# Kernel tuning notes

Hardware: AMD Instinct MI355X
Metric: run time of the kernel (lower is better)

The kernel has to match this reference:

```python
import jax, jax.numpy as jnp
import numpy as np
import math

D = 1024            # model dim
H = 4               # gru heads
HD = D // H         # 256 head dim
DI = int(HD * 1.5)  # 384 minGRU inner dim (expansion_factor=1.5)
FF_INNER = int(D * 4 * 2 / 3)  # 2730 SwiGLU inner
K = 4               # causal depthwise conv kernel
RES_SCALE = 1.0     # 1/sqrt(num_layers=1)


def setup_inputs() -> dict:
    key = jax.random.key(0)
    ks = jax.random.split(key, 12)
    s = lambda k, shape, sc: jax.random.normal(k, shape, jnp.float32) * sc
    return {
        "x": s(ks[0], (4, 4096, D), 1.0),
        "dw_w": s(ks[1], (D, 1, K), 0.3),
        "dw_b": jnp.zeros((D,), jnp.float32),
        "pw_w": s(ks[2], (D, D), 1.0 / math.sqrt(D)),
        "pw_b": jnp.zeros((D,), jnp.float32),
        "conv_gamma": jnp.zeros((D,), jnp.float32),
        "gru_gamma": jnp.zeros((D,), jnp.float32),
        "ff_gamma": jnp.zeros((D,), jnp.float32),
        "w_hg": s(ks[3], (H, HD, 2 * DI), 1.0 / math.sqrt(HD)),
        "w_out": s(ks[4], (H, DI, HD), 1.0 / math.sqrt(DI)),
        "w_gate": s(ks[5], (D, FF_INNER), 1.0 / math.sqrt(D)),
        "w_value": s(ks[6], (D, FF_INNER), 1.0 / math.sqrt(D)),
        "w_ff_out": s(ks[7], (FF_INNER, D), 1.0 / math.sqrt(FF_INNER)),
    }


def _rmsnorm(x, gamma):
    # F.normalize(x, dim=-1) * sqrt(dim) * (gamma + 1)
    n = jnp.sqrt(jnp.sum(x * x, axis=-1, keepdims=True))
    return x / jnp.maximum(n, 1e-12) * math.sqrt(x.shape[-1]) * (gamma + 1.0)


def _log_g(x):
    return jnp.where(x >= 0, jnp.log(jax.nn.relu(x) + 0.5), -jax.nn.softplus(-x))


def _causal_conv(x, dw_w, dw_b, pw_w, pw_b):
    # x: [B,L,D] -> causal depthwise conv (k=K) -> pointwise 1x1
    xt = jnp.transpose(x, (0, 2, 1))  # [B,D,L]
    xt = jnp.pad(xt, ((0, 0), (0, 0), (K - 1, 0)))
    y = jax.lax.conv_general_dilated(
        xt, dw_w, (1,), "VALID",
        dimension_numbers=("NCH", "OIH", "NCH"),
        feature_group_count=D) + dw_b[None, :, None]
    y = jnp.einsum("bdl,ed->bel", y, pw_w) + pw_b[None, :, None]
    return jnp.transpose(y, (0, 2, 1))


def reference(x, dw_w, dw_b, pw_w, pw_b, conv_gamma, gru_gamma, ff_gamma,
              w_hg, w_out, w_gate, w_value, w_ff_out):
    B, L, _ = x.shape
    # conv residual branch
    x = _causal_conv(_rmsnorm(x, conv_gamma), dw_w, dw_b, pw_w, pw_b) * RES_SCALE + x
    # multi-head minGRU (all heads vectorized; prev_hidden=None)
    normed = _rmsnorm(x, gru_gamma).reshape(B, L, H, HD)
    hg = jnp.einsum("blhd,hde->blhe", normed, w_hg)  # [B,L,H,2*DI]
    hidden, gate = hg[..., :DI], hg[..., DI:]
    log_coeffs = -jax.nn.softplus(gate)
    log_values = -jax.nn.softplus(-gate) + _log_g(hidden)
    # heinsen associative scan in log space along L
    a_star = jnp.cumsum(log_coeffs, axis=1)
    log_h = a_star + jax.lax.cumlogsumexp(log_values - a_star, axis=1)
    h = jnp.exp(log_h)  # [B,L,H,DI]
    next_hidden = h[:, -1:].reshape(B, 1, H * DI)
    gru_out = jnp.einsum("blhe,heo->blho", h, w_out).reshape(B, L, D)
    x = gru_out * RES_SCALE + x
    # SwiGLU FFN residual branch
    n = _rmsnorm(x, ff_gamma)
    ff = (jax.nn.silu(n @ w_gate) * (n @ w_value)) @ w_ff_out
    x = ff * RES_SCALE + x
    return x, next_hidden
```

## Files before the change

kernel.cpp:

```cpp
#include <hip/hip_runtime.h>
#include <stdint.h>


#define DM     1024
#define SEQL   4096
#define FFN    2730
#define FFP    2816
#define NH_OFF 16777216L
#define CHLEN  128

using bf16x8 = __attribute__((ext_vector_type(8))) short;
using f32x4  = __attribute__((ext_vector_type(4))) float;

__device__ __forceinline__ float bf2f(unsigned short h) {
  union { unsigned int u; float f; } v; v.u = ((unsigned int)h) << 16; return v.f;
}
__device__ __forceinline__ unsigned short f2bf(float f) {
  union { float f; unsigned int u; } v; v.f = f;
  unsigned int u = v.u;
  return (unsigned short)((u + 0x7fffu + ((u >> 16) & 1u)) >> 16);
}
__device__ __forceinline__ float ldin(const void* p, long i, int f32mode) {
  return f32mode ? ((const float*)p)[i] : bf2f(((const unsigned short*)p)[i]);
}
__device__ __forceinline__ void stout(void* p, long i, int f32mode, float v) {
  if (f32mode) ((float*)p)[i] = v; else ((unsigned short*)p)[i] = f2bf(v);
}
__device__ __forceinline__ void gload_lds16(const unsigned short* g, unsigned short* lds) {
  __builtin_amdgcn_global_load_lds(
      (const __attribute__((address_space(1))) unsigned int*)g,
      (__attribute__((address_space(3))) unsigned int*)lds,
      16, 0, 0);
}

__global__ void detect_k(const unsigned short* __restrict__ x, int* __restrict__ flag) {
  __shared__ int cnt;
  if (threadIdx.x == 0) cnt = 0;
  __syncthreads();
  int c = 0;
  for (int j = 0; j < 4; j++) {
    unsigned short v = x[2 * (threadIdx.x * 4 + j)];
    int ex = (v >> 7) & 0xFF;
    if (ex >= 0x84) c++;
  }
  atomicAdd(&cnt, c);
  __syncthreads();
  if (threadIdx.x == 0) *flag = (cnt >= 32) ? 1 : 0;
}

template <int EPI>
__launch_bounds__(256)
__global__ void gemm_bf16(const unsigned short* __restrict__ A, int lda, int aOffZ,
                          const unsigned short* __restrict__ Bm, int bOffZ, int K,
                          void* __restrict__ Cout, int ldc, int cOffZ, long outOff,
                          const unsigned short* __restrict__ bias,
                          const void* __restrict__ res, int ldres, long resOff,
                          const int* __restrict__ flagp) {
  __shared__ __align__(16) unsigned short As[128][64];
  __shared__ __align__(16) unsigned short Bs[128][64];

  const int tid  = threadIdx.x;
  const int w    = tid >> 6;
  const int lane = tid & 63;
  const int z    = blockIdx.z;
  const long tm  = (long)blockIdx.y * 128;
  const long tn  = (long)blockIdx.x * 128;

  const unsigned short* Ag = A + (long)z * aOffZ;
  const unsigned short* Bg = Bm + (long)z * bOffZ;

  f32x4 acc[4][4];
#pragma unroll
  for (int i = 0; i < 4; i++)
#pragma unroll
    for (int j = 0; j < 4; j++) acc[i][j] = (f32x4){0.f, 0.f, 0.f, 0.f};

  const int wrow = w * 32;
  const int srow = lane >> 3;
  const int scol = (((lane & 7) ^ srow) * 8);
  const int wm   = (w >> 1) * 64;
  const int wn   = (w & 1) * 64;
  const int quad = lane >> 4;
  const int lo   = lane & 15;
  const int sw   = lo & 7;

  for (int k0 = 0; k0 < K; k0 += 64) {
    __syncthreads();
#pragma unroll
    for (int i = 0; i < 4; i++) {
      const int r = wrow + i * 8;
      gload_lds16(Ag + (tm + r + srow) * (long)lda + k0 + scol, &As[r][0]);
      gload_lds16(Bg + (tn + r + srow) * (long)K + k0 + scol, &Bs[r][0]);
    }
    __syncthreads();
#pragma unroll
    for (int kk = 0; kk < 64; kk += 32) {
      const int kc = kk >> 3;
      bf16x8 af[4], bfr[4];
#pragma unroll
      for (int mt = 0; mt < 4; mt++)
        af[mt] = *(const bf16x8*)&As[wm + mt * 16 + lo][((quad + kc) ^ sw) * 8];
#pragma unroll
      for (int nt = 0; nt < 4; nt++)
        bfr[nt] = *(const bf16x8*)&Bs[wn + nt * 16 + lo][((quad + kc) ^ sw) * 8];
#pragma unroll
      for (int mt = 0; mt < 4; mt++)
#pragma unroll
        for (int nt = 0; nt < 4; nt++)
          acc[mt][nt] = __builtin_amdgcn_mfma_f32_16x16x32_bf16(af[mt], bfr[nt], acc[mt][nt], 0, 0, 0);
    }
  }

  const int f32m = (EPI == 1 || EPI == 3) ? *flagp : 0;
#pragma unroll
  for (int mt = 0; mt < 4; mt++) {
#pragma unroll
    for (int nt = 0; nt < 4; nt++) {
#pragma unroll
      for (int r = 0; r < 4; r++) {
        const long grow = tm + wm + mt * 16 + quad * 4 + r;
        const long gcol = tn + wn + nt * 16 + lo;
        float v         = acc[mt][nt][r];
        if (EPI == 0) {
          ((unsigned short*)Cout + (long)z * cOffZ)[grow * (long)ldc + gcol] = f2bf(v);
        } else if (EPI == 1) {
          v += bf2f(bias[gcol]) + ldin(res, resOff + grow * (long)ldres + gcol, f32m);
          ((unsigned short*)Cout)[grow * (long)ldc + gcol] = f2bf(v);
        } else if (EPI == 2) {
          v += bf2f(((const unsigned short*)res + (long)z * cOffZ)[grow * (long)ldres + gcol]);
          ((unsigned short*)Cout + (long)z * cOffZ)[grow * (long)ldc + gcol] = f2bf(v);
        } else {
          v += bf2f(((const unsigned short*)res)[grow * (long)ldres + gcol]);
          stout(Cout, outOff + grow * (long)ldc + gcol, f32m, v);
        }
      }
    }
  }
}

__launch_bounds__(256)
__global__ void gemm_ff(const unsigned short* __restrict__ A,
                        const unsigned short* __restrict__ Bgm,
                        const unsigned short* __restrict__ Bvm,
                        unsigned short* __restrict__ Cout) {
  __shared__ __align__(16) unsigned short As[128][64];
  __shared__ __align__(16) unsigned short Bgs[128][64];
  __shared__ __align__(16) unsigned short Bvs[128][64];

  const int tid  = threadIdx.x;
  const int w    = tid >> 6;
  const int lane = tid & 63;
  const long tm  = (long)blockIdx.y * 128;
  const long tn  = (long)blockIdx.x * 128;

  f32x4 accG[4][4], accV[4][4];
#pragma unroll
  for (int i = 0; i < 4; i++)
#pragma unroll
    for (int j = 0; j < 4; j++) {
      accG[i][j] = (f32x4){0.f, 0.f, 0.f, 0.f};
      accV[i][j] = (f32x4){0.f, 0.f, 0.f, 0.f};
    }

  const int wrow = w * 32;
  const int srow = lane >> 3;
  const int scol = (((lane & 7) ^ srow) * 8);
  const int wm   = (w >> 1) * 64;
  const int wn   = (w & 1) * 64;
  const int quad = lane >> 4;
  const int lo   = lane & 15;
  const int sw   = lo & 7;

  for (int k0 = 0; k0 < DM; k0 += 64) {
    __syncthreads();
#pragma unroll
    for (int i = 0; i < 4; i++) {
      const int r = wrow + i * 8;
      gload_lds16(A + (tm + r + srow) * (long)DM + k0 + scol, &As[r][0]);
      gload_lds16(Bgm + (tn + r + srow) * (long)DM + k0 + scol, &Bgs[r][0]);
      gload_lds16(Bvm + (tn + r + srow) * (long)DM + k0 + scol, &Bvs[r][0]);
    }
    __syncthreads();
#pragma unroll
    for (int kk = 0; kk < 64; kk += 32) {
      const int kc = kk >> 3;
      bf16x8 af[4], bfr[4];
#pragma unroll
      for (int mt = 0; mt < 4; mt++)
        af[mt] = *(const bf16x8*)&As[wm + mt * 16 + lo][((quad + kc) ^ sw) * 8];
#pragma unroll
      for (int nt = 0; nt < 4; nt++)
        bfr[nt] = *(const bf16x8*)&Bgs[wn + nt * 16 + lo][((quad + kc) ^ sw) * 8];
#pragma unroll
      for (int mt = 0; mt < 4; mt++)
#pragma unroll
        for (int nt = 0; nt < 4; nt++)
          accG[mt][nt] = __builtin_amdgcn_mfma_f32_16x16x32_bf16(af[mt], bfr[nt], accG[mt][nt], 0, 0, 0);
#pragma unroll
      for (int nt = 0; nt < 4; nt++)
        bfr[nt] = *(const bf16x8*)&Bvs[wn + nt * 16 + lo][((quad + kc) ^ sw) * 8];
#pragma unroll
      for (int mt = 0; mt < 4; mt++)
#pragma unroll
        for (int nt = 0; nt < 4; nt++)
          accV[mt][nt] = __builtin_amdgcn_mfma_f32_16x16x32_bf16(af[mt], bfr[nt], accV[mt][nt], 0, 0, 0);
    }
  }

#pragma unroll
  for (int mt = 0; mt < 4; mt++) {
#pragma unroll
    for (int nt = 0; nt < 4; nt++) {
#pragma unroll
      for (int r = 0; r < 4; r++) {
        const long grow = tm + wm + mt * 16 + quad * 4 + r;
        const long gcol = tn + wn + nt * 16 + lo;
        const float g   = accG[mt][nt][r];
        const float s   = g / (1.f + __expf(-g));
        Cout[grow * (long)FFP + gcol] = f2bf(s * accV[mt][nt][r]);
      }
    }
  }
}

template <int EPI>
__launch_bounds__(512, 2)
__global__ void gemm256(const unsigned short* __restrict__ A,
                        const unsigned short* __restrict__ Bm,
                        int K,
                        void* __restrict__ Cout,
                        const unsigned short* __restrict__ res,
                        long outOff,
                        const int* __restrict__ flagp) {
  __shared__ __align__(16) unsigned short As[2][256][64];
  __shared__ __align__(16) unsigned short Bs[2][256][64];

  const int tid  = threadIdx.x;
  const int w    = tid >> 6;
  const int lane = tid & 63;
  const int wr   = w >> 2;
  const int wc   = w & 3;
  const int quad = lane >> 4;
  const int lo   = lane & 15;
  const int sw   = lo & 7;

  const int gx  = gridDim.x;
  int bid       = blockIdx.y * gx + blockIdx.x;
  const int nwg = gx * gridDim.y;
  {
    const int q = nwg >> 3, r8 = nwg & 7;
    const int xc8 = bid & 7, j = bid >> 3;
    bid = (xc8 < r8 ? xc8 * (q + 1) : r8 * (q + 1) + (xc8 - r8) * q) + j;
  }
  const long tn = (long)(bid % gx) * 256;
  const long tm = (long)(bid / gx) * 256;

  const int NT = K >> 6;

  const int srow = lane >> 3;
  const int sch  = (lane & 7) ^ srow;
  const unsigned short* Ab = A + (tm + (long)w * 8 + srow) * (long)K + sch * 8;
  const unsigned short* Bb = Bm + (tn + (long)w * 8 + srow) * (long)K + sch * 8;

#define STAGE_A(BUF, TT, G) \
  gload_lds16(Ab + (long)((G) * 64) * K + (long)(TT) * 64, &As[BUF][(G) * 64 + w * 8][0])
#define STAGE_B(BUF, TT, G) \
  gload_lds16(Bb + (long)((G) * 64) * K + (long)(TT) * 64, &Bs[BUF][(G) * 64 + w * 8][0])

  STAGE_A(0, 0, 0); STAGE_A(0, 0, 2);
  STAGE_A(0, 0, 1); STAGE_A(0, 0, 3);
  STAGE_B(0, 0, 0); STAGE_B(0, 0, 1); STAGE_B(0, 0, 2); STAGE_B(0, 0, 3);
  STAGE_A(1, 1, 0); STAGE_A(1, 1, 2);
  STAGE_A(1, 1, 1); STAGE_A(1, 1, 3);
  STAGE_B(1, 1, 0); STAGE_B(1, 1, 1); STAGE_B(1, 1, 2); STAGE_B(1, 1, 3);

  f32x4 acc[8][4];
#pragma unroll
  for (int i = 0; i < 8; i++)
#pragma unroll
    for (int j = 0; j < 4; j++) acc[i][j] = (f32x4){0.f, 0.f, 0.f, 0.f};

  asm volatile("s_waitcnt vmcnt(8)" ::: "memory");
  __builtin_amdgcn_s_barrier();

  bf16x8 aL[4][2], aH[4][2], b01[2][2], b23[2][2];

#define LDAL(CBUF)                                                                \
  _Pragma("unroll") for (int m = 0; m < 4; m++) {                                 \
    _Pragma("unroll") for (int c = 0; c < 2; c++) {                               \
      aL[m][c] = *(const bf16x8*)&As[CBUF][wr * 128 + m * 16 + lo]                \
                                        [((quad + 4 * c) ^ sw) * 8];              \
    }                                                                             \
  }
#define LDAH(CBUF)                                                                \
  _Pragma("unroll") for (int m = 0; m < 4; m++) {                                 \
    _Pragma("unroll") for (int c = 0; c < 2; c++) {                               \
      aH[m][c] = *(const bf16x8*)&As[CBUF][wr * 128 + 64 + m * 16 + lo]           \
                                        [((quad + 4 * c) ^ sw) * 8];              \
    }                                                                             \
  }
#define LDB01(CBUF)                                                               \
  _Pragma("unroll") for (int n = 0; n < 2; n++) {                                 \
    _Pragma("unroll") for (int c = 0; c < 2; c++) {                               \
      b01[n][c] = *(const bf16x8*)&Bs[CBUF][wc * 64 + n * 16 + lo]                \
                                         [((quad + 4 * c) ^ sw) * 8];             \
    }                                                                             \
  }
#define LDB23(CBUF)                                                               \
  _Pragma("unroll") for (int n = 0; n < 2; n++) {                                 \
    _Pragma("unroll") for (int c = 0; c < 2; c++) {                               \
      b23[n][c] = *(const bf16x8*)&Bs[CBUF][wc * 64 + 32 + n * 16 + lo]           \
                                         [((quad + 4 * c) ^ sw) * 8];             \
    }                                                                             \
  }
#define MFMA_Q(MB, AF, NB, BF)                                                    \
  __builtin_amdgcn_s_setprio(1);                                                  \
  _Pragma("unroll") for (int m = 0; m < 4; m++) {                                 \
    _Pragma("unroll") for (int n = 0; n < 2; n++) {                               \
      _Pragma("unroll") for (int c = 0; c < 2; c++) {                             \
        acc[(MB) + m][(NB) + n] = __builtin_amdgcn_mfma_f32_16x16x32_bf16(        \
            AF[m][c], BF[n][c], acc[(MB) + m][(NB) + n], 0, 0, 0);                \
      }                                                                           \
    }                                                                             \
  }                                                                               \
  __builtin_amdgcn_s_setprio(0);

#define LGKM0 asm volatile("s_waitcnt lgkmcnt(0)" ::: "memory")

#define SUBTILE(CBUF, TT, STG, PRF, VM)                                           \
  {                                                                               \
                                                            \
    LGKM0;                                                                        \
    if (STG) { STAGE_A(CBUF, (TT) + 2, 0); STAGE_A(CBUF, (TT) + 2, 2); }          \
    MFMA_Q(0, aL, 0, b01);                                                        \
    LDAH(CBUF);                                                                   \
    __builtin_amdgcn_s_barrier();                                                 \
                                                            \
    LGKM0;                                                                        \
    if (STG) { STAGE_A(CBUF, (TT) + 2, 1); STAGE_A(CBUF, (TT) + 2, 3); }          \
    MFMA_Q(4, aH, 0, b01);                                                        \
    LDB23(CBUF);                                                                  \
    if ((VM) == 4) asm volatile("s_waitcnt vmcnt(4)" ::: "memory");               \
    else if ((VM) == 0) asm volatile("s_waitcnt vmcnt(0)" ::: "memory");          \
    __builtin_amdgcn_s_barrier();                                                 \
                                                            \
    LGKM0;                                                                        \
    if (STG) { STAGE_B(CBUF, (TT) + 2, 0); STAGE_B(CBUF, (TT) + 2, 1);            \
               STAGE_B(CBUF, (TT) + 2, 2); STAGE_B(CBUF, (TT) + 2, 3); }          \
    MFMA_Q(0, aL, 2, b23);                                                        \
    if (PRF) LDB01(CBUF ^ 1);                                                     \
    __builtin_amdgcn_s_barrier();                                                 \
                        \
    MFMA_Q(4, aH, 2, b23);                                                        \
    if (PRF) LDAL(CBUF ^ 1);                                                      \
    __builtin_amdgcn_s_barrier();                                                 \
  }

  LDB01(0);
  LDAL(0);

  for (int t = 0; t + 3 < NT; t += 2) {
    SUBTILE(0, t, 1, 1, 4)
    SUBTILE(1, t + 1, 1, 1, 4)
  }
  SUBTILE(0, NT - 2, 0, 1, 0)
  SUBTILE(1, NT - 1, 0, 0, -1)

  if (EPI == 0) {
    const long colb = (tn >> 1);
    const long rowb = tm + wr * 128;
#pragma unroll
    for (int m = 0; m < 8; m++) {
#pragma unroll
      for (int np = 0; np < 2; np++) {
        const long col = colb + (wc * 2 + np) * 16 + lo;
#pragma unroll
        for (int r = 0; r < 4; r++) {
          const long row = rowb + m * 16 + quad * 4 + r;
          const float g  = acc[m][2 * np][r];
          const float v  = acc[m][2 * np + 1][r];
          const float s  = g / (1.f + __expf(-g));
          ((unsigned short*)Cout)[row * (long)FFP + col] = f2bf(s * v);
        }
      }
    }
  } else {
    const int f32m = *flagp;
    const long rowb = tm + wr * 128;
    const long colb = tn + wc * 64;
#pragma unroll
    for (int m = 0; m < 8; m++) {
#pragma unroll
      for (int n = 0; n < 4; n++) {
#pragma unroll
        for (int r = 0; r < 4; r++) {
          const long row = rowb + m * 16 + quad * 4 + r;
          const long col = colb + n * 16 + lo;
          float v = acc[m][n][r] + bf2f(res[row * (long)DM + col]);
          stout(Cout, outOff + row * (long)DM + col, f32m, v);
        }
      }
    }
  }
#undef STAGE_A
#undef STAGE_B
#undef LDAL
#undef LDAH
#undef LDB01
#undef LDB23
#undef MFMA_Q
#undef LGKM0
#undef SUBTILE
}

__global__ void rmsnorm_x(const void* __restrict__ in, long elemOff,
                          const unsigned short* __restrict__ gamma,
                          unsigned short* __restrict__ out,
                          const int* __restrict__ flagp) {
  const int t    = blockIdx.x;
  const int lane = threadIdx.x;
  const int f32m = *flagp;
  float v[16];
  const long base = elemOff + (long)t * DM;
  if (f32m) {
    const float4* rp = (const float4*)((const float*)in + base);
#pragma unroll
    for (int j = 0; j < 4; j++) {
      float4 u     = rp[j * 64 + lane];
      v[j * 4 + 0] = u.x; v[j * 4 + 1] = u.y; v[j * 4 + 2] = u.z; v[j * 4 + 3] = u.w;
    }
  } else {
    const ushort4* rp = (const ushort4*)((const unsigned short*)in + base);
#pragma unroll
    for (int j = 0; j < 4; j++) {
      ushort4 u    = rp[j * 64 + lane];
      v[j * 4 + 0] = bf2f(u.x); v[j * 4 + 1] = bf2f(u.y);
      v[j * 4 + 2] = bf2f(u.z); v[j * 4 + 3] = bf2f(u.w);
    }
  }
  float s = 0.f;
#pragma unroll
  for (int i = 0; i < 16; i++) s = fmaf(v[i], v[i], s);
#pragma unroll
  for (int off = 32; off > 0; off >>= 1) s += __shfl_xor(s, off, 64);
  const float scale = 32.f / fmaxf(sqrtf(s), 1e-12f);
  ushort4* op       = (ushort4*)(out + (long)t * DM);
  const ushort4* gp = (const ushort4*)gamma;
#pragma unroll
  for (int j = 0; j < 4; j++) {
    ushort4 g = gp[j * 64 + lane];
    ushort4 o;
    o.x = f2bf(v[j * 4 + 0] * scale * (bf2f(g.x) + 1.f));
    o.y = f2bf(v[j * 4 + 1] * scale * (bf2f(g.y) + 1.f));
    o.z = f2bf(v[j * 4 + 2] * scale * (bf2f(g.z) + 1.f));
    o.w = f2bf(v[j * 4 + 3] * scale * (bf2f(g.w) + 1.f));
    op[j * 64 + lane] = o;
  }
}

__global__ void rmsnorm_k(const unsigned short* __restrict__ in,
                          const unsigned short* __restrict__ gamma,
                          unsigned short* __restrict__ out) {
  const int t    = blockIdx.x;
  const int lane = threadIdx.x;
  float v[16];
  const ushort4* rp = (const ushort4*)(in + (long)t * DM);
#pragma unroll
  for (int j = 0; j < 4; j++) {
    ushort4 u    = rp[j * 64 + lane];
    v[j * 4 + 0] = bf2f(u.x); v[j * 4 + 1] = bf2f(u.y);
    v[j * 4 + 2] = bf2f(u.z); v[j * 4 + 3] = bf2f(u.w);
  }
  float s = 0.f;
#pragma unroll
  for (int i = 0; i < 16; i++) s = fmaf(v[i], v[i], s);
#pragma unroll
  for (int off = 32; off > 0; off >>= 1) s += __shfl_xor(s, off, 64);
  const float scale = 32.f / fmaxf(sqrtf(s), 1e-12f);
  ushort4* op       = (ushort4*)(out + (long)t * DM);
  const ushort4* gp = (const ushort4*)gamma;
#pragma unroll
  for (int j = 0; j < 4; j++) {
    ushort4 g = gp[j * 64 + lane];
    ushort4 o;
    o.x = f2bf(v[j * 4 + 0] * scale * (bf2f(g.x) + 1.f));
    o.y = f2bf(v[j * 4 + 1] * scale * (bf2f(g.y) + 1.f));
    o.z = f2bf(v[j * 4 + 2] * scale * (bf2f(g.z) + 1.f));
    o.w = f2bf(v[j * 4 + 3] * scale * (bf2f(g.w) + 1.f));
    op[j * 64 + lane] = o;
  }
}

__global__ void dwconv_k(const unsigned short* __restrict__ xn,
                         const unsigned short* __restrict__ dww,
                         const unsigned short* __restrict__ dwb,
                         unsigned short* __restrict__ y, int l0) {
  const int t = blockIdx.x;
  const int d = blockIdx.y * 256 + threadIdx.x;
  const int l = l0 + (t & (SEQL - 1));
  ushort4 w4  = ((const ushort4*)dww)[d];
  float wk[4] = {bf2f(w4.x), bf2f(w4.y), bf2f(w4.z), bf2f(w4.w)};
  float acc   = bf2f(dwb[d]);
#pragma unroll
  for (int k = 0; k < 4; k++) {
    const int ll = l + k - 3;
    if (ll >= 0) acc = fmaf(bf2f(xn[(long)(t + k - 3) * DM + d]), wk[k], acc);
  }
  y[(long)t * DM + d] = f2bf(acc);
}

__device__ __forceinline__ void cv_compute(float gt, float& c, float& sg) {
  gt = fminf(fmaxf(gt, -40.f), 40.f);
  const float e  = __expf(-fabsf(gt));
  const float r  = 1.f / (1.f + e);
  const float rs = e * r;
  c  = (gt >= 0.f) ? rs : r;
  sg = (gt >= 0.f) ? r : rs;
}
__device__ __forceinline__ float gfun(float hid) {
  hid = fminf(fmaxf(hid, -40.f), 40.f);
  if (hid >= 0.f) return hid + 0.5f;
  const float e = __expf(hid);
  return e / (1.f + e);
}

__global__ void scan_p1(const unsigned short* __restrict__ hg, float* __restrict__ cC,
                        float* __restrict__ cV, int chTot, int SL) {
  const int e = threadIdx.x, bh = blockIdx.y, cid = blockIdx.x;
  const int bL = bh >> 2, hh = bh & 3;
  long base = ((long)(bL * SL + cid * CHLEN)) * 3072 + hh * 768 + e;
  float C = 1.f, V = 0.f;
  for (int i = 0; i < CHLEN; i++) {
    const float hid = bf2f(hg[base]), gt = bf2f(hg[base + 384]);
    float c, sg; cv_compute(gt, c, sg);
    C *= c;
    V = fmaf(c, V, sg * gfun(hid));
    base += 3072;
  }
  const int idx = cid * chTot + bh * 384 + e;
  cC[idx] = C; cV[idx] = V;
}

__global__ void scan_p2(const float* __restrict__ cC, const float* __restrict__ cV,
                        float* __restrict__ hin, int chTot, int CHNp,
                        const float* __restrict__ hcarry, int useCarry) {
  const int ch = blockIdx.x * 384 + threadIdx.x;
  float h = useCarry ? hcarry[ch] : 0.f;
  for (int cid = 0; cid < CHNp; cid++) {
    const int idx = cid * chTot + ch;
    hin[idx] = h;
    h = fmaf(cC[idx], h, cV[idx]);
  }
}

__global__ void scan_p3(const unsigned short* __restrict__ hg, const float* __restrict__ hin,
                        unsigned short* __restrict__ hout, void* __restrict__ nh, long nhOff,
                        float* __restrict__ hcarry, int chTot, int SL, int CHNp,
                        int writeNh, const int* __restrict__ flagp) {
  const int e = threadIdx.x, bh = blockIdx.y, cid = blockIdx.x;
  const int bL = bh >> 2, hh = bh & 3;
  const long tok = (long)bL * SL + (long)cid * CHLEN;
  long base  = tok * 3072 + hh * 768 + e;
  long obase = tok * 1536 + hh * 384 + e;
  float h = hin[cid * chTot + bh * 384 + e];
  for (int i = 0; i < CHLEN; i++) {
    const float hid = bf2f(hg[base]), gt = bf2f(hg[base + 384]);
    float c, sg; cv_compute(gt, c, sg);
    h = fmaf(c, h, sg * gfun(hid));
    hout[obase] = f2bf(h);
    base += 3072; obase += 1536;
  }
  if (cid == CHNp - 1) {
    hcarry[bh * 384 + e] = h;
    if (writeNh) stout(nh, nhOff + bL * 1536 + hh * 384 + e, *flagp, h);
  }
}

__global__ void cvt_k(const void* __restrict__ in, unsigned short* __restrict__ out,
                      int n, const int* __restrict__ flagp) {
  const int i = blockIdx.x * 256 + threadIdx.x;
  if (i < n) out[i] = f2bf(ldin(in, i, *flagp));
}
__global__ void tr_whg(const void* __restrict__ in, unsigned short* __restrict__ out,
                       const int* __restrict__ flagp) {
  const int idx = blockIdx.x * 256 + threadIdx.x;
  const int k = idx & 255, n = (idx >> 8) % 768, h = idx / (768 * 256);
  out[idx] = f2bf(ldin(in, (long)(h * 256 + k) * 768 + n, *flagp));
}
__global__ void tr_wout(const void* __restrict__ in, unsigned short* __restrict__ out,
                        const int* __restrict__ flagp) {
  const int idx = blockIdx.x * 256 + threadIdx.x;
  const int k = idx % 384, n = (idx / 384) & 255, h = idx / (384 * 256);
  out[idx] = f2bf(ldin(in, (long)(h * 384 + k) * 256 + n, *flagp));
}
__global__ void tr_wg(const void* __restrict__ in, unsigned short* __restrict__ out,
                      const int* __restrict__ flagp) {
  const int idx = blockIdx.x * 256 + threadIdx.x;
  const int k = idx & 1023, n = idx >> 10;
  out[idx] = (n < FFN) ? f2bf(ldin(in, (long)k * FFN + n, *flagp)) : (unsigned short)0;
}
__global__ void tr_wgv(const void* __restrict__ wg, const void* __restrict__ wv,
                       unsigned short* __restrict__ out, const int* __restrict__ flagp) {
  const int idx = blockIdx.x * 256 + threadIdx.x;
  const int k = idx & 1023, R = idx >> 10;
  const int tile = R >> 8, rb = R & 255;
  const int pair = rb >> 5, sel = (rb >> 4) & 1, r16 = rb & 15;
  const int col  = tile * 128 + pair * 16 + r16;
  const void* src = sel ? wv : wg;
  out[idx] = (col < FFN) ? f2bf(ldin(src, (long)k * FFN + col, *flagp)) : (unsigned short)0;
}
__global__ void tr_wfo(const void* __restrict__ in, unsigned short* __restrict__ out,
                       const int* __restrict__ flagp) {
  const int idx = blockIdx.x * 256 + threadIdx.x;
  const int kk = idx % FFP, n = idx / FFP;
  out[idx] = (kk < FFN) ? f2bf(ldin(in, (long)kk * DM + n, *flagp)) : (unsigned short)0;
}

extern "C" void kernel_launch(void* const* d_in, const int* in_sizes, int n_in,
                              void* d_out, int out_size, void* d_ws, size_t ws_size,
                              hipStream_t stream) {
  const void* x      = d_in[0];
  const void* dw_w   = d_in[1];
  const void* dw_b   = d_in[2];
  const void* pw_w   = d_in[3];
  const void* pw_b   = d_in[4];
  const void* conv_g = d_in[5];
  const void* gru_g  = d_in[6];
  const void* ff_g   = d_in[7];
  const void* w_hg   = d_in[8];
  const void* w_out  = d_in[9];
  const void* w_gate = d_in[10];
  const void* w_val  = d_in[11];
  const void* w_ffo  = d_in[12];

  const long FIXED = 21795072L;
  int MT = 128;
  if      (ws_size >= (size_t)(FIXED + 16384L * 13888)) MT = 16384;
  else if (ws_size >= (size_t)(FIXED + 8192L * 13888))  MT = 8192;
  else if (ws_size >= (size_t)(FIXED + 4096L * 13888))  MT = 4096;
  else if (ws_size >= (size_t)(FIXED + 2048L * 13888))  MT = 2048;
  else if (ws_size >= (size_t)(FIXED + 1024L * 13888))  MT = 1024;
  else if (ws_size >= (size_t)(FIXED + 512L * 13888))   MT = 512;
  else if (ws_size >= (size_t)(FIXED + 256L * 13888))   MT = 256;

  const int SL    = (MT >= SEQL) ? SEQL : MT;
  const int nSeq  = MT / SL;
  const int CHNp  = SL / CHLEN;
  const int chTot = nSeq * 1536;
  const int big   = (MT >= 256);

  char* p = (char*)d_ws;
  unsigned short* whgT  = (unsigned short*)p; p += 1572864;
  unsigned short* woutT = (unsigned short*)p; p += 786432;
  unsigned short* wgT   = (unsigned short*)p; p += 5767168;
  unsigned short* wvT   = (unsigned short*)p; p += 5767168;
  unsigned short* wfoT  = (unsigned short*)p; p += 5767168;
  unsigned short* pwT   = (unsigned short*)p; p += 2097152;
  unsigned short* dwwB  = (unsigned short*)p; p += 8192;
  unsigned short* dwbB  = (unsigned short*)p; p += 2048;
  unsigned short* pwbB  = (unsigned short*)p; p += 2048;
  unsigned short* cgB   = (unsigned short*)p; p += 2048;
  unsigned short* ggB   = (unsigned short*)p; p += 2048;
  unsigned short* fgB   = (unsigned short*)p; p += 2048;
  int*            flag  = (int*)p;            p += 256;
  float*          hcarry= (float*)p;          p += 12288;
  float*          cC    = (float*)p;          p += (long)MT * 192;
  float*          cV    = (float*)p;          p += (long)MT * 192;
  float*          hin   = (float*)p;          p += (long)MT * 192;
  unsigned short* xnb   = (unsigned short*)p; p += 6144 + (long)MT * 2048;
  unsigned short* xc    = (unsigned short*)p; p += (long)MT * 2048;
  unsigned short* hbuf  = (unsigned short*)p; p += (long)MT * 3072;
  unsigned short* ybuf  = (unsigned short*)p;
  unsigned short* hg    = (unsigned short*)p;
  unsigned short* ffin  = (unsigned short*)p;
  unsigned short* xn    = xnb + 3 * DM;
  unsigned short* wgvT  = wgT;

  detect_k<<<1, 256, 0, stream>>>((const unsigned short*)x, flag);
  tr_whg<<<3072, 256, 0, stream>>>(w_hg, whgT, flag);
  tr_wout<<<1536, 256, 0, stream>>>(w_out, woutT, flag);
  if (big) {
    tr_wgv<<<22528, 256, 0, stream>>>(w_gate, w_val, wgvT, flag);
  } else {
    tr_wg<<<11264, 256, 0, stream>>>(w_gate, wgT, flag);
    tr_wg<<<11264, 256, 0, stream>>>(w_val, wvT, flag);
  }
  tr_wfo<<<11264, 256, 0, stream>>>(w_ffo, wfoT, flag);
  cvt_k<<<4096, 256, 0, stream>>>(pw_w, pwT, 1048576, flag);
  cvt_k<<<16, 256, 0, stream>>>(dw_w, dwwB, 4096, flag);
  cvt_k<<<4, 256, 0, stream>>>(dw_b, dwbB, 1024, flag);
  cvt_k<<<4, 256, 0, stream>>>(pw_b, pwbB, 1024, flag);
  cvt_k<<<4, 256, 0, stream>>>(conv_g, cgB, 1024, flag);
  cvt_k<<<4, 256, 0, stream>>>(gru_g, ggB, 1024, flag);
  cvt_k<<<4, 256, 0, stream>>>(ff_g, fgB, 1024, flag);

  for (long t0 = 0; t0 < 16384; t0 += MT) {
    const int l0     = (int)(t0 & (SEQL - 1));
    const int P      = (l0 > 0) ? 3 : 0;
    const int seqEnd = (l0 + SL == SEQL);
    const long nhOff = NH_OFF + (t0 / SEQL) * 1536;

    rmsnorm_x<<<MT + P, 64, 0, stream>>>(x, (t0 - P) * DM, cgB, xn - (long)P * DM, flag);
    dwconv_k<<<dim3(MT, 4), 256, 0, stream>>>(xn, dwwB, dwbB, ybuf, l0);
    gemm_bf16<1><<<dim3(8, MT / 128, 1), 256, 0, stream>>>(ybuf, DM, 0, pwT, 0, DM,
        xc, DM, 0, 0L, pwbB, x, DM, t0 * DM, flag);

    rmsnorm_k<<<MT, 64, 0, stream>>>(xc, ggB, xn);
    gemm_bf16<0><<<dim3(6, MT / 128, 4), 256, 0, stream>>>(xn, DM, 256, whgT, 196608, 256,
        hg, 3072, 768, 0L, nullptr, nullptr, 0, 0L, nullptr);
    scan_p1<<<dim3(CHNp, nSeq * 4), 384, 0, stream>>>(hg, cC, cV, chTot, SL);
    scan_p2<<<nSeq * 4, 384, 0, stream>>>(cC, cV, hin, chTot, CHNp, hcarry, l0 > 0);
    scan_p3<<<dim3(CHNp, nSeq * 4), 384, 0, stream>>>(hg, hin, hbuf, d_out, nhOff,
        hcarry, chTot, SL, CHNp, seqEnd, flag);
    gemm_bf16<2><<<dim3(2, MT / 128, 4), 256, 0, stream>>>(hbuf, 1536, 384, woutT, 98304, 384,
        xc, DM, 256, 0L, nullptr, xc, DM, 0L, nullptr);

    rmsnorm_k<<<MT, 64, 0, stream>>>(xc, fgB, xn);
    if (big) {
      gemm256<0><<<dim3(22, MT / 256), 512, 0, stream>>>(xn, wgvT, DM,
          ffin, nullptr, 0L, nullptr);
      gemm256<1><<<dim3(4, MT / 256), 512, 0, stream>>>(ffin, wfoT, FFP,
          d_out, xc, t0 * DM, flag);
    } else {
      gemm_ff<<<dim3(22, MT / 128), 256, 0, stream>>>(xn, wgT, wvT, ffin);
      gemm_bf16<3><<<dim3(8, MT / 128, 1), 256, 0, stream>>>(ffin, FFP, 0, wfoT, 0, FFP,
          d_out, DM, 0, t0 * DM, nullptr, xc, DM, 0L, flag);
    }
  }
}
```

Before: 1.063 ms.

## Restructure GEMM subtile schedule: reorder LDS loads, staging and MFMA quadrants

Reworks the inner-loop schedule of the 256x256 bf16 GEMM. The cross-subtile register prefetch of the next buffer's A/B fragments and the explicit lgkmcnt(0) waits are removed. LDS fragment loads are now issued at the start of each subtile, B and A global->LDS staging are each grouped into one phase, and the vmcnt wait threshold is changed to 8. The aim is cleaner overlap of global staging with MFMA, but dropping the register prefetch exposes more LDS latency at subtile starts, and removing the explicit waits puts correctness at the mercy of compiler-inserted waits.

Measured after the change: 966.4 us. 1.1x faster.

```diff
diff --git a/kernel.cpp b/kernel.cpp
--- a/kernel.cpp
+++ b/kernel.cpp
@@ -267,12 +267,10 @@
 #define STAGE_B(BUF, TT, G) \
   gload_lds16(Bb + (long)((G) * 64) * K + (long)(TT) * 64, &Bs[BUF][(G) * 64 + w * 8][0])
 
-  STAGE_A(0, 0, 0); STAGE_A(0, 0, 2);
-  STAGE_A(0, 0, 1); STAGE_A(0, 0, 3);
+  STAGE_A(0, 0, 0); STAGE_A(0, 0, 1); STAGE_A(0, 0, 2); STAGE_A(0, 0, 3);
   STAGE_B(0, 0, 0); STAGE_B(0, 0, 1); STAGE_B(0, 0, 2); STAGE_B(0, 0, 3);
-  STAGE_A(1, 1, 0); STAGE_A(1, 1, 2);
-  STAGE_A(1, 1, 1); STAGE_A(1, 1, 3);
   STAGE_B(1, 1, 0); STAGE_B(1, 1, 1); STAGE_B(1, 1, 2); STAGE_B(1, 1, 3);
+  STAGE_A(1, 1, 0); STAGE_A(1, 1, 1); STAGE_A(1, 1, 2); STAGE_A(1, 1, 3);
 
   f32x4 acc[8][4];
 #pragma unroll
@@ -325,46 +323,38 @@
   }                                                                               \
   __builtin_amdgcn_s_setprio(0);
 
-#define LGKM0 asm volatile("s_waitcnt lgkmcnt(0)" ::: "memory")
-
-#define SUBTILE(CBUF, TT, STG, PRF, VM)                                           \
+#define SUBTILE(CBUF, TT, STG, VM)                                                \
   {                                                                               \
-                                                            \
-    LGKM0;                                                                        \
-    if (STG) { STAGE_A(CBUF, (TT) + 2, 0); STAGE_A(CBUF, (TT) + 2, 2); }          \
+         \
+    LDAL(CBUF);                                                                   \
+    LDB01(CBUF);                                                                  \
     MFMA_Q(0, aL, 0, b01);                                                        \
+    LDB23(CBUF);                                                                  \
+    __builtin_amdgcn_s_barrier();                                                 \
+                      \
+    MFMA_Q(0, aL, 2, b23);                                                        \
+    __builtin_amdgcn_s_barrier();                                                 \
+         \
+    if (STG) { STAGE_B(CBUF, (TT) + 2, 0); STAGE_B(CBUF, (TT) + 2, 1);            \
+               STAGE_B(CBUF, (TT) + 2, 2); STAGE_B(CBUF, (TT) + 2, 3); }          \
     LDAH(CBUF);                                                                   \
+    MFMA_Q(4, aH, 2, b23);                                                        \
     __builtin_amdgcn_s_barrier();                                                 \
-                                                            \
-    LGKM0;                                                                        \
-    if (STG) { STAGE_A(CBUF, (TT) + 2, 1); STAGE_A(CBUF, (TT) + 2, 3); }          \
+         \
+    if (STG) { STAGE_A(CBUF, (TT) + 2, 0); STAGE_A(CBUF, (TT) + 2, 1);            \
+               STAGE_A(CBUF, (TT) + 2, 2); STAGE_A(CBUF, (TT) + 2, 3); }          \
     MFMA_Q(4, aH, 0, b01);                                                        \
-    LDB23(CBUF);                                                                  \
-    if ((VM) == 4) asm volatile("s_waitcnt vmcnt(4)" ::: "memory");               \
+    if ((VM) == 8) asm volatile("s_waitcnt vmcnt(8)" ::: "memory");               \
     else if ((VM) == 0) asm volatile("s_waitcnt vmcnt(0)" ::: "memory");          \
     __builtin_amdgcn_s_barrier();                                                 \
-                                                            \
-    LGKM0;                                                                        \
-    if (STG) { STAGE_B(CBUF, (TT) + 2, 0); STAGE_B(CBUF, (TT) + 2, 1);            \
-               STAGE_B(CBUF, (TT) + 2, 2); STAGE_B(CBUF, (TT) + 2, 3); }          \
-    MFMA_Q(0, aL, 2, b23);                                                        \
-    if (PRF) LDB01(CBUF ^ 1);                                                     \
-    __builtin_amdgcn_s_barrier();                                                 \
-                        \
-    MFMA_Q(4, aH, 2, b23);                                                        \
-    if (PRF) LDAL(CBUF ^ 1);                                                      \
-    __builtin_amdgcn_s_barrier();                                                 \
-  }
-
-  LDB01(0);
-  LDAL(0);
+  }
 
   for (int t = 0; t + 3 < NT; t += 2) {
-    SUBTILE(0, t, 1, 1, 4)
-    SUBTILE(1, t + 1, 1, 1, 4)
-  }
-  SUBTILE(0, NT - 2, 0, 1, 0)
-  SUBTILE(1, NT - 1, 0, 0, -1)
+    SUBTILE(0, t, 1, 8)
+    SUBTILE(1, t + 1, 1, 8)
+  }
+  SUBTILE(0, NT - 2, 0, 0)
+  SUBTILE(1, NT - 1, 0, -1)
 
   if (EPI == 0) {
     const long colb = (tn >> 1);
@@ -409,7 +399,6 @@
 #undef LDB01
 #undef LDB23
 #undef MFMA_Q
-#undef LGKM0
 #undef SUBTILE
 }
 
```

## Reschedule GEMM main-loop phases to interleave LDS reads with MFMA

Applied to the files above, without the earlier changes.

Reorders the four-phase schedule of the bf16 MFMA GEMM main loop. Both B fragment halves are now loaded up front, the A-high fragment loads are split into two halves spread across phases, and the global-to-LDS staging of each buffer region is moved to phases where no wave still reads it. The explicit lgkmcnt(0) waits are replaced by sched_barrier plus s_barrier phase boundaries, and the prologue issue order and vmcnt thresholds are adjusted to match. The aim is to hide LDS read latency behind MFMA work. This relies on the compiler to insert the LDS waits and raises register pressure from holding more fragments at once.

After: 1.056 ms. No clear change (-0.7%).

```diff
diff --git a/kernel.cpp b/kernel.cpp
--- a/kernel.cpp
+++ b/kernel.cpp
@@ -268,11 +268,11 @@
   gload_lds16(Bb + (long)((G) * 64) * K + (long)(TT) * 64, &Bs[BUF][(G) * 64 + w * 8][0])
 
   STAGE_A(0, 0, 0); STAGE_A(0, 0, 2);
+  STAGE_B(0, 0, 0); STAGE_B(0, 0, 1); STAGE_B(0, 0, 2); STAGE_B(0, 0, 3);
   STAGE_A(0, 0, 1); STAGE_A(0, 0, 3);
-  STAGE_B(0, 0, 0); STAGE_B(0, 0, 1); STAGE_B(0, 0, 2); STAGE_B(0, 0, 3);
   STAGE_A(1, 1, 0); STAGE_A(1, 1, 2);
+  STAGE_B(1, 1, 0); STAGE_B(1, 1, 1); STAGE_B(1, 1, 2); STAGE_B(1, 1, 3);
   STAGE_A(1, 1, 1); STAGE_A(1, 1, 3);
-  STAGE_B(1, 1, 0); STAGE_B(1, 1, 1); STAGE_B(1, 1, 2); STAGE_B(1, 1, 3);
 
   f32x4 acc[8][4];
 #pragma unroll
@@ -292,8 +292,15 @@
                                         [((quad + 4 * c) ^ sw) * 8];              \
     }                                                                             \
   }
-#define LDAH(CBUF)                                                                \
-  _Pragma("unroll") for (int m = 0; m < 4; m++) {                                 \
+#define LDAH1(CBUF)                                                               \
+  _Pragma("unroll") for (int m = 0; m < 2; m++) {                                 \
+    _Pragma("unroll") for (int c = 0; c < 2; c++) {                               \
+      aH[m][c] = *(const bf16x8*)&As[CBUF][wr * 128 + 64 + m * 16 + lo]           \
+                                        [((quad + 4 * c) ^ sw) * 8];              \
+    }                                                                             \
+  }
+#define LDAH2(CBUF)                                                               \
+  _Pragma("unroll") for (int m = 2; m < 4; m++) {                                 \
     _Pragma("unroll") for (int c = 0; c < 2; c++) {                               \
       aH[m][c] = *(const bf16x8*)&As[CBUF][wr * 128 + 64 + m * 16 + lo]           \
                                         [((quad + 4 * c) ^ sw) * 8];              \
@@ -325,43 +332,46 @@
   }                                                                               \
   __builtin_amdgcn_s_setprio(0);
 
-#define LGKM0 asm volatile("s_waitcnt lgkmcnt(0)" ::: "memory")
+#define PHASE_END                                                                 \
+  __builtin_amdgcn_sched_barrier(0);                                              \
+  __builtin_amdgcn_s_barrier();
 
 #define SUBTILE(CBUF, TT, STG, PRF, VM)                                           \
   {                                                                               \
-                                                            \
-    LGKM0;                                                                        \
+     \
+     \
+    LDB01(CBUF);                                                                  \
+    LDB23(CBUF);                                                                  \
+    MFMA_Q(0, aL, 0, b01);                                                        \
+    PHASE_END;                                                                    \
+     \
+     \
     if (STG) { STAGE_A(CBUF, (TT) + 2, 0); STAGE_A(CBUF, (TT) + 2, 2); }          \
-    MFMA_Q(0, aL, 0, b01);                                                        \
-    LDAH(CBUF);                                                                   \
-    __builtin_amdgcn_s_barrier();                                                 \
-                                                            \
-    LGKM0;                                                                        \
-    if (STG) { STAGE_A(CBUF, (TT) + 2, 1); STAGE_A(CBUF, (TT) + 2, 3); }          \
-    MFMA_Q(4, aH, 0, b01);                                                        \
-    LDB23(CBUF);                                                                  \
-    if ((VM) == 4) asm volatile("s_waitcnt vmcnt(4)" ::: "memory");               \
-    else if ((VM) == 0) asm volatile("s_waitcnt vmcnt(0)" ::: "memory");          \
-    __builtin_amdgcn_s_barrier();                                                 \
-                                                            \
-    LGKM0;                                                                        \
+    LDAH1(CBUF);                                                                  \
+    MFMA_Q(0, aL, 2, b23);                                                        \
+    PHASE_END;                                                                    \
+     \
+     \
     if (STG) { STAGE_B(CBUF, (TT) + 2, 0); STAGE_B(CBUF, (TT) + 2, 1);            \
                STAGE_B(CBUF, (TT) + 2, 2); STAGE_B(CBUF, (TT) + 2, 3); }          \
-    MFMA_Q(0, aL, 2, b23);                                                        \
-    if (PRF) LDB01(CBUF ^ 1);                                                     \
-    __builtin_amdgcn_s_barrier();                                                 \
-                        \
+    LDAH2(CBUF);                                                                  \
     MFMA_Q(4, aH, 2, b23);                                                        \
+    if ((VM) == 6) asm volatile("s_waitcnt vmcnt(6)" ::: "memory");               \
+    else if ((VM) == 0) asm volatile("s_waitcnt vmcnt(0)" ::: "memory");          \
+    PHASE_END;                                                                    \
+     \
+     \
+    if (STG) { STAGE_A(CBUF, (TT) + 2, 1); STAGE_A(CBUF, (TT) + 2, 3); }          \
     if (PRF) LDAL(CBUF ^ 1);                                                      \
-    __builtin_amdgcn_s_barrier();                                                 \
-  }
-
-  LDB01(0);
+    MFMA_Q(4, aH, 0, b01);                                                        \
+    PHASE_END;                                                                    \
+  }
+
   LDAL(0);
 
   for (int t = 0; t + 3 < NT; t += 2) {
-    SUBTILE(0, t, 1, 1, 4)
-    SUBTILE(1, t + 1, 1, 1, 4)
+    SUBTILE(0, t, 1, 1, 6)
+    SUBTILE(1, t + 1, 1, 1, 6)
   }
   SUBTILE(0, NT - 2, 0, 1, 0)
   SUBTILE(1, NT - 1, 0, 0, -1)
@@ -405,11 +415,12 @@
 #undef STAGE_A
 #undef STAGE_B
 #undef LDAL
-#undef LDAH
+#undef LDAH1
+#undef LDAH2
 #undef LDB01
 #undef LDB23
 #undef MFMA_Q
-#undef LGKM0
+#undef PHASE_END
 #undef SUBTILE
 }
 
```
